# Kernel tuning notes

Measured on AMD Instinct MI355X. Metric: run time of the kernel, lower is better.

The kernel has to match this reference:

```python
import jax, jax.numpy as jnp
import numpy as np

B, N, D, K = 1024, 8192, 256, 8
LAMBDA_MULT = 0.01

def setup_inputs() -> dict:
    key = jax.random.key(0)
    k1, k2, k3, k4, k5 = jax.random.split(key, 5)
    x = jax.random.uniform(k1, (B, D), dtype=jnp.float32)
    mu = jax.random.uniform(k2, (N, D), dtype=jnp.float32)
    lambda_base = jax.random.uniform(k3, (N,), dtype=jnp.float32) * LAMBDA_MULT
    v = jax.random.normal(k4, (N, K, D), dtype=jnp.float32)  # stands in for per-unit orthogonal init
    omega = 0.1 + 0.4 * jax.random.uniform(k5, (N, K), dtype=jnp.float32)
    return {"x": x, "mu": mu, "lambda_base": lambda_base, "v": v, "omega": omega}

def reference(x, mu, lambda_base, v, omega):
    # quad_form = diff^T (lambda*I + sum_k omega_k v_k v_k^T) diff
    #           = lambda * ||x - mu||^2 + sum_k omega_k * ((x - mu) . v_k)^2
    # Woodbury-style expansion avoids materializing W:(n,d,d) and diff:(b,n,d).
    x2 = jnp.sum(x * x, axis=-1)                      # (b,)
    mu2 = jnp.sum(mu * mu, axis=-1)                   # (n,)
    xm = x @ mu.T                                     # (b,n)
    sqdist = x2[:, None] - 2.0 * xm + mu2[None, :]    # (b,n) = ||x-mu||^2
    xv = jnp.einsum('bd,nkd->bnk', x, v)              # (b,n,k)
    muv = jnp.einsum('nd,nkd->nk', mu, v)             # (n,k)
    proj2 = (xv - muv[None, :, :]) ** 2               # (b,n,k)
    quad = lambda_base[None, :] * sqdist + jnp.einsum('bnk,nk->bn', proj2, omega)
    return jnp.exp(-quad / D)  # Type == 'exp'
```

## Files before the change

### kernel.cpp

```cpp
#include <hip/hip_runtime.h>


#define B_SZ 1024
#define N_SZ 8192
#define D_SZ 256
#define K_SZ 8

#define BT 128
#define NT 16
#define LDS_STRIDE 40

typedef __bf16 bf16x8 __attribute__((ext_vector_type(8)));
typedef float f32x4 __attribute__((ext_vector_type(4)));
typedef unsigned short u16x8 __attribute__((ext_vector_type(8)));

__device__ __forceinline__ float wave_reduce(float s) {
#pragma unroll
  for (int off = 32; off > 0; off >>= 1) s += __shfl_down(s, off);
  return s;
}

__global__ void p1_x2(const float* __restrict__ x, float* __restrict__ x2) {
  const int b = blockIdx.x, l = threadIdx.x;
  const float* xr = x + (size_t)b * D_SZ;
  float s = 0.f;
#pragma unroll
  for (int i = 0; i < 4; ++i) { float f = xr[l + 64 * i]; s += f * f; }
  s = wave_reduce(s);
  if (l == 0) x2[b] = s;
}

__global__ void p2_mu(const float* __restrict__ mu, const float* __restrict__ v,
                      float* __restrict__ mu2, float* __restrict__ muv) {
  const int n = blockIdx.x, l = threadIdx.x;
  const float* mr = mu + (size_t)n * D_SZ;
  float md[4];
  float m2 = 0.f;
#pragma unroll
  for (int i = 0; i < 4; ++i) { md[i] = mr[l + 64 * i]; m2 += md[i] * md[i]; }
  m2 = wave_reduce(m2);
  if (l == 0) mu2[n] = m2;
#pragma unroll
  for (int k = 0; k < K_SZ; ++k) {
    const float* vr = v + (size_t)(n * K_SZ + k) * D_SZ;
    float s = 0.f;
#pragma unroll
    for (int i = 0; i < 4; ++i) s += md[i] * vr[l + 64 * i];
    s = wave_reduce(s);
    if (l == 0) muv[n * K_SZ + k] = s;
  }
}

__device__ __forceinline__ void cvt16_store(const float* __restrict__ src,
                                            unsigned short* dst ) {
  const float4* p4 = (const float4*)src;
  float fv[16];
#pragma unroll
  for (int e = 0; e < 4; ++e) {
    float4 t = p4[e];
    fv[4 * e + 0] = t.x; fv[4 * e + 1] = t.y;
    fv[4 * e + 2] = t.z; fv[4 * e + 3] = t.w;
  }
  u16x8 lo, hi;
#pragma unroll
  for (int e = 0; e < 8; ++e) {
    lo[e] = __builtin_bit_cast(unsigned short, (__bf16)fv[e]);
    hi[e] = __builtin_bit_cast(unsigned short, (__bf16)fv[e + 8]);
  }
  *(u16x8*)dst = lo;
  *(u16x8*)(dst + 8) = hi;
}

__global__ __launch_bounds__(256, 2)
void hmu_main(const float* __restrict__ x, const float* __restrict__ mu,
              const float* __restrict__ lam, const float* __restrict__ v,
              const float* __restrict__ om, const float* __restrict__ ws,
              float* __restrict__ out) {
  __shared__ __align__(16) unsigned short As[BT * LDS_STRIDE];
  __shared__ __align__(16) unsigned short Bs[NT * 9 * LDS_STRIDE];

  const float* ws_x2 = ws;
  const float* ws_mu2 = ws + B_SZ;
  const float* ws_muv = ws + B_SZ + N_SZ;

  const int tid = threadIdx.x;
  const int lane = tid & 63;
  const int w = tid >> 6;
  const int m = lane & 15;
  const int kg = lane >> 4;

  const int n0 = blockIdx.x * NT;
  const int b0 = blockIdx.y * BT;

  f32x4 acc[2][9];
#pragma unroll
  for (int bs = 0; bs < 2; ++bs)
#pragma unroll
    for (int j = 0; j < 9; ++j) acc[bs][j] = (f32x4){0.f, 0.f, 0.f, 0.f};

  const int arow = tid >> 1, ahalf = tid & 1;

  for (int kt = 0; kt < 8; ++kt) {
    const int k0 = kt * 32;
    cvt16_store(x + (size_t)(b0 + arow) * D_SZ + k0 + ahalf * 16,
                &As[arow * LDS_STRIDE + ahalf * 16]);
#pragma unroll
    for (int it = 0; it < 2; ++it) {
      int idx = tid + 256 * it;
      if (idx < 288) {
        int row = idx >> 1, half = idx & 1;
        int nl = row / 9;
        int j = row - nl * 9;
        const float* src = (j == 0)
            ? mu + (size_t)(n0 + nl) * D_SZ + k0 + half * 16
            : v + (size_t)((n0 + nl) * K_SZ + (j - 1)) * D_SZ + k0 + half * 16;
        cvt16_store(src, &Bs[row * LDS_STRIDE + half * 16]);
      }
    }
    __syncthreads();

    bf16x8 af[2];
#pragma unroll
    for (int bs = 0; bs < 2; ++bs) {
      int r = (2 * w + bs) * 16 + m;
      af[bs] = *(const bf16x8*)&As[r * LDS_STRIDE + kg * 8];
    }
#pragma unroll
    for (int j = 0; j < 9; ++j) {
      bf16x8 bfr = *(const bf16x8*)&Bs[(m * 9 + j) * LDS_STRIDE + kg * 8];
      acc[0][j] = __builtin_amdgcn_mfma_f32_16x16x32_bf16(af[0], bfr, acc[0][j], 0, 0, 0);
      acc[1][j] = __builtin_amdgcn_mfma_f32_16x16x32_bf16(af[1], bfr, acc[1][j], 0, 0, 0);
    }
    __syncthreads();
  }

  const int n = n0 + m;
  const float lam_n = lam[n];
  const float mu2_n = ws_mu2[n];
  float omr[8], muvr[8];
#pragma unroll
  for (int k = 0; k < 8; ++k) {
    omr[k] = om[n * 8 + k];
    muvr[k] = ws_muv[n * 8 + k];
  }
#pragma unroll
  for (int bs = 0; bs < 2; ++bs) {
#pragma unroll
    for (int r = 0; r < 4; ++r) {
      int b = b0 + (2 * w + bs) * 16 + kg * 4 + r;
      float x2b = ws_x2[b];
      float c0 = acc[bs][0][r];
      float q = lam_n * (x2b - 2.f * c0 + mu2_n);
#pragma unroll
      for (int k = 0; k < 8; ++k) {
        float p = acc[bs][k + 1][r] - muvr[k];
        q = fmaf(omr[k] * p, p, q);
      }
      out[(size_t)b * N_SZ + n] = __expf(q * (-1.0f / 256.0f));
    }
  }
}

extern "C" void kernel_launch(void* const* d_in, const int* in_sizes, int n_in,
                              void* d_out, int out_size, void* d_ws, size_t ws_size,
                              hipStream_t stream) {
  const float* x   = (const float*)d_in[0];
  const float* mu  = (const float*)d_in[1];
  const float* lam = (const float*)d_in[2];
  const float* v   = (const float*)d_in[3];
  const float* om  = (const float*)d_in[4];
  float* out = (float*)d_out;
  float* ws  = (float*)d_ws;

  p1_x2<<<B_SZ, 64, 0, stream>>>(x, ws);
  p2_mu<<<N_SZ, 64, 0, stream>>>(mu, v, ws + B_SZ, ws + B_SZ + N_SZ);
  dim3 grid(N_SZ / NT, B_SZ / BT);
  hmu_main<<<grid, 256, 0, stream>>>(x, mu, lam, v, om, ws, out);
}
```

Baseline: 196.6 us.

## Double batch tile to 256 rows and vectorize precompute kernels

The main kernel's batch tile grows from 128 to 256 rows, so each wave computes four 16-row MFMA subtiles per B fragment instead of two. This halves how often the mu and v tiles are reloaded and converted across blocks, but doubles the accumulator registers (36 f32x4) and LDS for A, which may hurt occupancy under launch_bounds(256,2). The x2 and mu/muv precompute kernels now use float4 loads, with four waves per block sharing work and mu staged in LDS.

```diff
diff --git a/kernel.cpp b/kernel.cpp
--- a/kernel.cpp
+++ b/kernel.cpp
@@ -6,7 +6,7 @@
 #define D_SZ 256
 #define K_SZ 8
 
-#define BT 128
+#define BT 256
 #define NT 16
 #define LDS_STRIDE 40
 
@@ -21,33 +21,35 @@
 }
 
 __global__ void p1_x2(const float* __restrict__ x, float* __restrict__ x2) {
-  const int b = blockIdx.x, l = threadIdx.x;
-  const float* xr = x + (size_t)b * D_SZ;
-  float s = 0.f;
-#pragma unroll
-  for (int i = 0; i < 4; ++i) { float f = xr[l + 64 * i]; s += f * f; }
+  const int w = threadIdx.x >> 6, lane = threadIdx.x & 63;
+  const int b = blockIdx.x * 4 + w;
+  float4 t = *(const float4*)(x + (size_t)b * D_SZ + 4 * lane);
+  float s = t.x * t.x + t.y * t.y + t.z * t.z + t.w * t.w;
   s = wave_reduce(s);
-  if (l == 0) x2[b] = s;
+  if (lane == 0) x2[b] = s;
 }
 
 __global__ void p2_mu(const float* __restrict__ mu, const float* __restrict__ v,
                       float* __restrict__ mu2, float* __restrict__ muv) {
-  const int n = blockIdx.x, l = threadIdx.x;
-  const float* mr = mu + (size_t)n * D_SZ;
-  float md[4];
-  float m2 = 0.f;
+  __shared__ __align__(16) float mulds[D_SZ];
+  const int n = blockIdx.x;
+  const int w = threadIdx.x >> 6, lane = threadIdx.x & 63;
+  if (w == 0) {
+    float4 m4 = *(const float4*)(mu + (size_t)n * D_SZ + 4 * lane);
+    *(float4*)(mulds + 4 * lane) = m4;
+    float s = m4.x * m4.x + m4.y * m4.y + m4.z * m4.z + m4.w * m4.w;
+    s = wave_reduce(s);
+    if (lane == 0) mu2[n] = s;
+  }
+  __syncthreads();
+  float4 m4 = *(const float4*)(mulds + 4 * lane);
 #pragma unroll
-  for (int i = 0; i < 4; ++i) { md[i] = mr[l + 64 * i]; m2 += md[i] * md[i]; }
-  m2 = wave_reduce(m2);
-  if (l == 0) mu2[n] = m2;
-#pragma unroll
-  for (int k = 0; k < K_SZ; ++k) {
-    const float* vr = v + (size_t)(n * K_SZ + k) * D_SZ;
-    float s = 0.f;
-#pragma unroll
-    for (int i = 0; i < 4; ++i) s += md[i] * vr[l + 64 * i];
+  for (int kk = 0; kk < 2; ++kk) {
+    const int k = w * 2 + kk;
+    float4 v4 = *(const float4*)(v + ((size_t)n * K_SZ + k) * D_SZ + 4 * lane);
+    float s = m4.x * v4.x + m4.y * v4.y + m4.z * v4.z + m4.w * v4.w;
     s = wave_reduce(s);
-    if (l == 0) muv[n * K_SZ + k] = s;
+    if (lane == 0) muv[n * K_SZ + k] = s;
   }
 }
 
@@ -92,18 +94,21 @@
   const int n0 = blockIdx.x * NT;
   const int b0 = blockIdx.y * BT;
 
-  f32x4 acc[2][9];
+  f32x4 acc[4][9];
 #pragma unroll
-  for (int bs = 0; bs < 2; ++bs)
+  for (int bs = 0; bs < 4; ++bs)
 #pragma unroll
     for (int j = 0; j < 9; ++j) acc[bs][j] = (f32x4){0.f, 0.f, 0.f, 0.f};
 
-  const int arow = tid >> 1, ahalf = tid & 1;
-
   for (int kt = 0; kt < 8; ++kt) {
     const int k0 = kt * 32;
-    cvt16_store(x + (size_t)(b0 + arow) * D_SZ + k0 + ahalf * 16,
-                &As[arow * LDS_STRIDE + ahalf * 16]);
+#pragma unroll
+    for (int it = 0; it < 2; ++it) {
+      int idx = tid + 256 * it;
+      int row = idx >> 1, half = idx & 1;
+      cvt16_store(x + (size_t)(b0 + row) * D_SZ + k0 + half * 16,
+                  &As[row * LDS_STRIDE + half * 16]);
+    }
 #pragma unroll
     for (int it = 0; it < 2; ++it) {
       int idx = tid + 256 * it;
@@ -119,17 +124,18 @@
     }
     __syncthreads();
 
-    bf16x8 af[2];
+    bf16x8 af[4];
 #pragma unroll
-    for (int bs = 0; bs < 2; ++bs) {
-      int r = (2 * w + bs) * 16 + m;
+    for (int bs = 0; bs < 4; ++bs) {
+      int r = (4 * w + bs) * 16 + m;
       af[bs] = *(const bf16x8*)&As[r * LDS_STRIDE + kg * 8];
     }
 #pragma unroll
     for (int j = 0; j < 9; ++j) {
       bf16x8 bfr = *(const bf16x8*)&Bs[(m * 9 + j) * LDS_STRIDE + kg * 8];
-      acc[0][j] = __builtin_amdgcn_mfma_f32_16x16x32_bf16(af[0], bfr, acc[0][j], 0, 0, 0);
-      acc[1][j] = __builtin_amdgcn_mfma_f32_16x16x32_bf16(af[1], bfr, acc[1][j], 0, 0, 0);
+#pragma unroll
+      for (int bs = 0; bs < 4; ++bs)
+        acc[bs][j] = __builtin_amdgcn_mfma_f32_16x16x32_bf16(af[bs], bfr, acc[bs][j], 0, 0, 0);
     }
     __syncthreads();
   }
@@ -144,10 +150,10 @@
     muvr[k] = ws_muv[n * 8 + k];
   }
 #pragma unroll
-  for (int bs = 0; bs < 2; ++bs) {
+  for (int bs = 0; bs < 4; ++bs) {
 #pragma unroll
     for (int r = 0; r < 4; ++r) {
-      int b = b0 + (2 * w + bs) * 16 + kg * 4 + r;
+      int b = b0 + (4 * w + bs) * 16 + kg * 4 + r;
       float x2b = ws_x2[b];
       float c0 = acc[bs][0][r];
       float q = lam_n * (x2b - 2.f * c0 + mu2_n);
@@ -172,8 +178,8 @@
   float* out = (float*)d_out;
   float* ws  = (float*)d_ws;
 
-  p1_x2<<<B_SZ, 64, 0, stream>>>(x, ws);
-  p2_mu<<<N_SZ, 64, 0, stream>>>(mu, v, ws + B_SZ, ws + B_SZ + N_SZ);
+  p1_x2<<<B_SZ / 4, 256, 0, stream>>>(x, ws);
+  p2_mu<<<N_SZ, 256, 0, stream>>>(mu, v, ws + B_SZ, ws + B_SZ + N_SZ);
   dim3 grid(N_SZ / NT, B_SZ / BT);
   hmu_main<<<grid, 256, 0, stream>>>(x, mu, lam, v, om, ws, out);
 }
```

After: 203.7 us. 3.6% more time.
